# Kernel optimization log

Hardware: AMD Instinct MI355X
Metric: run time of the kernel (lower is better)

Reference implementation:

```python
import jax, jax.numpy as jnp
from jax import lax
import numpy as np

B, T, F, H, C = 2048, 200, 64, 128, 1
IN = 2 * F + H  # GRUCell input size


def setup_inputs() -> dict:
    key = jax.random.key(0)
    ks = jax.random.split(key, 16)
    sd_h = 1.0 / np.sqrt(H)
    sd_f = 1.0 / np.sqrt(F)
    sd_g = 1.0 / np.sqrt(H)
    return {
        "values": jax.random.normal(ks[0], (B, T, F), jnp.float32),
        "masks": jnp.round(jax.random.uniform(ks[1], (B, T, F), jnp.float32)),
        "deltas": jax.random.uniform(ks[2], (B, T, F), jnp.float32),
        "x_locf": jax.random.normal(ks[3], (B, T, F), jnp.float32),
        "emp_mean": jax.random.normal(ks[4], (F,), jnp.float32),
        "Wdh": jax.random.uniform(ks[5], (H, F), jnp.float32, -sd_h, sd_h),
        "bdh": jax.random.uniform(ks[6], (H,), jnp.float32, -sd_h, sd_h),
        "Wdx": jax.random.uniform(ks[7], (F, F), jnp.float32, -sd_f, sd_f),
        "bdx": jax.random.uniform(ks[8], (F,), jnp.float32, -sd_f, sd_f),
        "w_ih": jax.random.uniform(ks[9], (3 * H, IN), jnp.float32, -sd_g, sd_g),
        "w_hh": jax.random.uniform(ks[10], (3 * H, H), jnp.float32, -sd_g, sd_g),
        "b_ih": jax.random.uniform(ks[11], (3 * H,), jnp.float32, -sd_g, sd_g),
        "b_hh": jax.random.uniform(ks[12], (3 * H,), jnp.float32, -sd_g, sd_g),
        "Wc": jax.random.uniform(ks[13], (C, H), jnp.float32, -sd_g, sd_g),
        "bc": jax.random.uniform(ks[14], (C,), jnp.float32, -sd_g, sd_g),
    }


def reference(values, masks, deltas, x_locf, emp_mean,
              Wdh, bdh, Wdx, bdx, w_ih, w_hh, b_ih, b_hh, Wc, bc):
    # GRU-D forward: sequential scan over time with temporal decay gating.
    eye = jnp.eye(Wdx.shape[0], dtype=Wdx.dtype)
    Wdx_diag = Wdx * eye  # diag=True TemporalDecay

    def step(h, inp):
        x, m, d, xl = inp  # each [B, F]
        gamma_h = jnp.exp(-jax.nn.relu(d @ Wdh.T + bdh))   # [B, H]
        gamma_x = jnp.exp(-jax.nn.relu(d @ Wdx_diag.T + bdx))  # [B, F]
        h = h * gamma_h
        x_h = gamma_x * xl + (1.0 - gamma_x) * emp_mean
        x_rep = m * x + (1.0 - m) * x_h
        inputs = jnp.concatenate([x_rep, h, m], axis=1)    # [B, 2F+H]
        gi = inputs @ w_ih.T + b_ih                        # [B, 3H]
        gh = h @ w_hh.T + b_hh                             # [B, 3H]
        i_r, i_z, i_n = jnp.split(gi, 3, axis=1)
        h_r, h_z, h_n = jnp.split(gh, 3, axis=1)
        r = jax.nn.sigmoid(i_r + h_r)
        z = jax.nn.sigmoid(i_z + h_z)
        n = jnp.tanh(i_n + r * h_n)
        h_new = (1.0 - z) * n + z * h
        return h_new, None

    xs = (values.transpose(1, 0, 2), masks.transpose(1, 0, 2),
          deltas.transpose(1, 0, 2), x_locf.transpose(1, 0, 2))
    h0 = jnp.zeros((values.shape[0], Wdh.shape[0]), values.dtype)
    h_final, _ = lax.scan(step, h0, xs)
    logits = h_final @ Wc.T + bc
    return jax.nn.sigmoid(logits)
```

## Files before the change

### kernel.cpp

```cpp
#include <hip/hip_runtime.h>
#include <hip/hip_bf16.h>

#define Bsz 2048
#define Tn  200
#define Fn  64
#define Hn  128
#define INn 256
#define BBn 8

typedef __bf16 bf16x8 __attribute__((ext_vector_type(8)));
typedef float  f32x4  __attribute__((ext_vector_type(4)));

__device__ __forceinline__ float sigm(float x)  { return 1.f / (1.f + __expf(-x)); }
__device__ __forceinline__ float tanh_(float x) { return 1.f - 2.f / (__expf(2.f * x) + 1.f); }

__global__ __launch_bounds__(512, 2) void grud_scan(
    const float* __restrict__ values, const float* __restrict__ masks,
    const float* __restrict__ deltas, const float* __restrict__ x_locf,
    const float* __restrict__ emp_mean,
    const float* __restrict__ Wdh, const float* __restrict__ bdh,
    const float* __restrict__ Wdx, const float* __restrict__ bdx,
    const float* __restrict__ w_ih, const float* __restrict__ w_hh,
    const float* __restrict__ b_ih, const float* __restrict__ b_hh,
    const float* __restrict__ Wc, const float* __restrict__ bc,
    float* __restrict__ out)
{
    __shared__ __align__(16) __bf16 in_bf[16][264];
    __shared__ __align__(16) __bf16 d_bf[2][16][72];
    __shared__ float h_fin[BBn][Hn];

    const int tid  = threadIdx.x;
    const int w    = tid >> 6;
    const int lane = tid & 63;
    const int ncol = lane & 15;
    const int kg   = lane >> 4;
    const int b0   = blockIdx.x * BBn;

    for (int i = tid; i < 16 * 264;    i += 512) ((__bf16*)in_bf)[i] = (__bf16)0.f;
    for (int i = tid; i < 2 * 16 * 72; i += 512) ((__bf16*)d_bf)[i]  = (__bf16)0.f;

    bf16x8 wih[3][8], whh[3][4], wdhf[2];
    float bih_r[3], bhh_r[3];
    #pragma unroll
    for (int nt = 0; nt < 3; ++nt) {
        const int c = nt * Hn + w * 16 + ncol;
        bih_r[nt] = b_ih[c];
        bhh_r[nt] = b_hh[c];
        #pragma unroll
        for (int kc = 0; kc < 8; ++kc) {
            const float* p = w_ih + (size_t)c * INn + kc * 32 + kg * 8;
            bf16x8 v;
            #pragma unroll
            for (int e = 0; e < 8; ++e) v[e] = (__bf16)p[e];
            wih[nt][kc] = v;
        }
        #pragma unroll
        for (int kc = 0; kc < 4; ++kc) {
            const float* p = w_hh + (size_t)c * Hn + kc * 32 + kg * 8;
            bf16x8 v;
            #pragma unroll
            for (int e = 0; e < 8; ++e) v[e] = (__bf16)p[e];
            whh[nt][kc] = v;
        }
    }
    const int ch = w * 16 + ncol;
    const float bdh_r = bdh[ch];
    #pragma unroll
    for (int kc = 0; kc < 2; ++kc) {
        const float* p = Wdh + (size_t)ch * Fn + kc * 32 + kg * 8;
        bf16x8 v;
        #pragma unroll
        for (int e = 0; e < 8; ++e) v[e] = (__bf16)p[e];
        wdhf[kc] = v;
    }

    const int r_ld = w, f_ld = lane;
    const float wdxd_r = Wdx[(size_t)f_ld * Fn + f_ld];
    const float bdx_r  = bdx[f_ld];
    const float emp_r  = emp_mean[f_ld];
    const float* vp = values + (size_t)(b0 + r_ld) * Tn * Fn + f_ld;
    const float* mp = masks  + (size_t)(b0 + r_ld) * Tn * Fn + f_ld;
    const float* dp = deltas + (size_t)(b0 + r_ld) * Tn * Fn + f_ld;
    const float* lp = x_locf + (size_t)(b0 + r_ld) * Tn * Fn + f_ld;

    float h_reg[4] = {0.f, 0.f, 0.f, 0.f};

    float x_c = vp[0], m_c = mp[0], d_c = dp[0], xl_c = lp[0];
    d_bf[0][r_ld][f_ld] = (__bf16)d_c;
    __syncthreads();

    const f32x4 fz = {0.f, 0.f, 0.f, 0.f};

    for (int t = 0; t < Tn; ++t) {
        const int cur = t & 1;

        bf16x8 a0 = *(const bf16x8*)&d_bf[cur][ncol][kg * 8];
        bf16x8 a1 = *(const bf16x8*)&d_bf[cur][ncol][32 + kg * 8];
        f32x4 acc = fz;
        acc = __builtin_amdgcn_mfma_f32_16x16x32_bf16(a0, wdhf[0], acc, 0, 0, 0);
        acc = __builtin_amdgcn_mfma_f32_16x16x32_bf16(a1, wdhf[1], acc, 0, 0, 0);
        if (kg < 2) {
            #pragma unroll
            for (int i = 0; i < 4; ++i) {
                float g  = __expf(-fmaxf(acc[i] + bdh_r, 0.f));
                float hv = h_reg[i] * g;
                h_reg[i] = hv;
                in_bf[kg * 4 + i][Fn + ch] = (__bf16)hv;
            }
        }
        {
            float gx = __expf(-fmaxf(d_c * wdxd_r + bdx_r, 0.f));
            float xh = gx * xl_c + (1.f - gx) * emp_r;
            float xr = m_c * x_c + (1.f - m_c) * xh;
            in_bf[r_ld][f_ld]            = (__bf16)xr;
            in_bf[r_ld][Fn + Hn + f_ld]  = (__bf16)m_c;
        }
        const int off = (t + 1 < Tn) ? (t + 1) * Fn : t * Fn;
        float x_n = vp[off], m_n = mp[off], d_n = dp[off], xl_n = lp[off];
        __syncthreads();

        bf16x8 af[8];
        #pragma unroll
        for (int kc = 0; kc < 8; ++kc)
            af[kc] = *(const bf16x8*)&in_bf[ncol][kc * 32 + kg * 8];
        f32x4 gacc[3], hacc[3];
        #pragma unroll
        for (int nt = 0; nt < 3; ++nt) { gacc[nt] = fz; hacc[nt] = fz; }
        #pragma unroll
        for (int kc = 0; kc < 8; ++kc)
            #pragma unroll
            for (int nt = 0; nt < 3; ++nt)
                gacc[nt] = __builtin_amdgcn_mfma_f32_16x16x32_bf16(af[kc], wih[nt][kc], gacc[nt], 0, 0, 0);
        #pragma unroll
        for (int kc = 0; kc < 4; ++kc)
            #pragma unroll
            for (int nt = 0; nt < 3; ++nt)
                hacc[nt] = __builtin_amdgcn_mfma_f32_16x16x32_bf16(af[kc + 2], whh[nt][kc], hacc[nt], 0, 0, 0);
        if (kg < 2) {
            #pragma unroll
            for (int i = 0; i < 4; ++i) {
                float rg = sigm(gacc[0][i] + bih_r[0] + hacc[0][i] + bhh_r[0]);
                float zg = sigm(gacc[1][i] + bih_r[1] + hacc[1][i] + bhh_r[1]);
                float hn = hacc[2][i] + bhh_r[2];
                float ng = tanh_(gacc[2][i] + bih_r[2] + rg * hn);
                h_reg[i] = (1.f - zg) * ng + zg * h_reg[i];
            }
        }
        x_c = x_n; m_c = m_n; d_c = d_n; xl_c = xl_n;
        d_bf[cur ^ 1][r_ld][f_ld] = (__bf16)d_n;
        __syncthreads();
    }

    if (kg < 2) {
        #pragma unroll
        for (int i = 0; i < 4; ++i) h_fin[kg * 4 + i][ch] = h_reg[i];
    }
    __syncthreads();
    if (tid < BBn) {
        float acc = bc[0];
        #pragma unroll 8
        for (int j = 0; j < Hn; ++j) acc += h_fin[tid][j] * Wc[j];
        out[b0 + tid] = sigm(acc);
    }
}

extern "C" void kernel_launch(void* const* d_in, const int* in_sizes, int n_in,
                              void* d_out, int out_size, void* d_ws, size_t ws_size,
                              hipStream_t stream)
{
    (void)in_sizes; (void)n_in; (void)out_size; (void)d_ws; (void)ws_size;
    grud_scan<<<dim3(Bsz / BBn), dim3(512), 0, stream>>>(
        (const float*)d_in[0],  (const float*)d_in[1],  (const float*)d_in[2],
        (const float*)d_in[3],  (const float*)d_in[4],  (const float*)d_in[5],
        (const float*)d_in[6],  (const float*)d_in[7],  (const float*)d_in[8],
        (const float*)d_in[9],  (const float*)d_in[10], (const float*)d_in[11],
        (const float*)d_in[12], (const float*)d_in[13], (const float*)d_in[14],
        (float*)d_out);
}
```

Measured before the change: 621.5 us.

## Fold W_hh r/z weights into W_ih and double-buffer LDS to drop a barrier

Because h appears in both the input concatenation and the hidden matmul, the r and z rows of w_hh are pre-added into the matching w_ih columns. This removes eight MFMAs per step, and only the n-gate hidden product stays separate. The input tile is double-buffered and the decay matmul for the next step is computed one step ahead, so each iteration needs one barrier instead of two. Summing weights before the bf16 conversion changes rounding slightly, and the single-barrier scheme relies on careful buffer alternation.

```diff
diff --git a/kernel.cpp b/kernel.cpp
--- a/kernel.cpp
+++ b/kernel.cpp
@@ -25,7 +25,7 @@
     const float* __restrict__ Wc, const float* __restrict__ bc,
     float* __restrict__ out)
 {
-    __shared__ __align__(16) __bf16 in_bf[16][264];
+    __shared__ __align__(16) __bf16 in_bf[2][16][264];
     __shared__ __align__(16) __bf16 d_bf[2][16][72];
     __shared__ float h_fin[BBn][Hn];
 
@@ -36,10 +36,10 @@
     const int kg   = lane >> 4;
     const int b0   = blockIdx.x * BBn;
 
-    for (int i = tid; i < 16 * 264;    i += 512) ((__bf16*)in_bf)[i] = (__bf16)0.f;
-    for (int i = tid; i < 2 * 16 * 72; i += 512) ((__bf16*)d_bf)[i]  = (__bf16)0.f;
+    for (int i = tid; i < 2 * 16 * 264; i += 512) ((__bf16*)in_bf)[i] = (__bf16)0.f;
+    for (int i = tid; i < 2 * 16 * 72;  i += 512) ((__bf16*)d_bf)[i]  = (__bf16)0.f;
 
-    bf16x8 wih[3][8], whh[3][4], wdhf[2];
+    bf16x8 wih[3][8], whn[4], wdhf[2];
     float bih_r[3], bhh_r[3];
     #pragma unroll
     for (int nt = 0; nt < 3; ++nt) {
@@ -49,18 +49,23 @@
         #pragma unroll
         for (int kc = 0; kc < 8; ++kc) {
             const float* p = w_ih + (size_t)c * INn + kc * 32 + kg * 8;
+            const bool fold = (nt < 2) & (kc >= 2) & (kc < 6);
+            const float* q = w_hh + (size_t)c * Hn + (kc - 2) * 32 + kg * 8;
             bf16x8 v;
             #pragma unroll
-            for (int e = 0; e < 8; ++e) v[e] = (__bf16)p[e];
+            for (int e = 0; e < 8; ++e) v[e] = (__bf16)(p[e] + (fold ? q[e] : 0.f));
             wih[nt][kc] = v;
         }
+    }
+    {
+        const int cn = 2 * Hn + w * 16 + ncol;
         #pragma unroll
         for (int kc = 0; kc < 4; ++kc) {
-            const float* p = w_hh + (size_t)c * Hn + kc * 32 + kg * 8;
+            const float* q = w_hh + (size_t)cn * Hn + kc * 32 + kg * 8;
             bf16x8 v;
             #pragma unroll
-            for (int e = 0; e < 8; ++e) v[e] = (__bf16)p[e];
-            whh[nt][kc] = v;
+            for (int e = 0; e < 8; ++e) v[e] = (__bf16)q[e];
+            whn[kc] = v;
         }
     }
     const int ch = w * 16 + ncol;
@@ -73,6 +78,8 @@
         for (int e = 0; e < 8; ++e) v[e] = (__bf16)p[e];
         wdhf[kc] = v;
     }
+    const float bs0 = bih_r[0] + bhh_r[0];
+    const float bs1 = bih_r[1] + bhh_r[1];
 
     const int r_ld = w, f_ld = lane;
     const float wdxd_r = Wdx[(size_t)f_ld * Fn + f_ld];
@@ -84,48 +91,60 @@
     const float* lp = x_locf + (size_t)(b0 + r_ld) * Tn * Fn + f_ld;
 
     float h_reg[4] = {0.f, 0.f, 0.f, 0.f};
-
-    float x_c = vp[0], m_c = mp[0], d_c = dp[0], xl_c = lp[0];
-    d_bf[0][r_ld][f_ld] = (__bf16)d_c;
-    __syncthreads();
-
     const f32x4 fz = {0.f, 0.f, 0.f, 0.f};
 
+    float x_c = vp[0], m_c = mp[0], xl_c = lp[0];
+    float d_cur = dp[0];
+    float d_w   = dp[Fn];
+    d_bf[1][r_ld][f_ld] = (__bf16)d_cur;
+    __syncthreads();
+    f32x4 gam = fz;
+    {
+        bf16x8 g0 = *(const bf16x8*)&d_bf[1][ncol][kg * 8];
+        bf16x8 g1 = *(const bf16x8*)&d_bf[1][ncol][32 + kg * 8];
+        gam = __builtin_amdgcn_mfma_f32_16x16x32_bf16(g0, wdhf[0], gam, 0, 0, 0);
+        gam = __builtin_amdgcn_mfma_f32_16x16x32_bf16(g1, wdhf[1], gam, 0, 0, 0);
+    }
+
     for (int t = 0; t < Tn; ++t) {
-        const int cur = t & 1;
+        const int buf = t & 1;
 
-        bf16x8 a0 = *(const bf16x8*)&d_bf[cur][ncol][kg * 8];
-        bf16x8 a1 = *(const bf16x8*)&d_bf[cur][ncol][32 + kg * 8];
-        f32x4 acc = fz;
-        acc = __builtin_amdgcn_mfma_f32_16x16x32_bf16(a0, wdhf[0], acc, 0, 0, 0);
-        acc = __builtin_amdgcn_mfma_f32_16x16x32_bf16(a1, wdhf[1], acc, 0, 0, 0);
+        const int o1 = (t + 1 < Tn ? t + 1 : Tn - 1) * Fn;
+        const int o2 = (t + 2 < Tn ? t + 2 : Tn - 1) * Fn;
+        const float x_n = vp[o1], m_n = mp[o1], xl_n = lp[o1], d_nn = dp[o2];
+
         if (kg < 2) {
             #pragma unroll
             for (int i = 0; i < 4; ++i) {
-                float g  = __expf(-fmaxf(acc[i] + bdh_r, 0.f));
-                float hv = h_reg[i] * g;
-                h_reg[i] = hv;
-                in_bf[kg * 4 + i][Fn + ch] = (__bf16)hv;
+                float g = __expf(-fmaxf(gam[i] + bdh_r, 0.f));
+                h_reg[i] *= g;
+                in_bf[buf][kg * 4 + i][Fn + ch] = (__bf16)h_reg[i];
             }
         }
         {
-            float gx = __expf(-fmaxf(d_c * wdxd_r + bdx_r, 0.f));
+            float gx = __expf(-fmaxf(d_cur * wdxd_r + bdx_r, 0.f));
             float xh = gx * xl_c + (1.f - gx) * emp_r;
             float xr = m_c * x_c + (1.f - m_c) * xh;
-            in_bf[r_ld][f_ld]            = (__bf16)xr;
-            in_bf[r_ld][Fn + Hn + f_ld]  = (__bf16)m_c;
+            in_bf[buf][r_ld][f_ld]           = (__bf16)xr;
+            in_bf[buf][r_ld][Fn + Hn + f_ld] = (__bf16)m_c;
+            d_bf[buf][r_ld][f_ld]            = (__bf16)d_w;
         }
-        const int off = (t + 1 < Tn) ? (t + 1) * Fn : t * Fn;
-        float x_n = vp[off], m_n = mp[off], d_n = dp[off], xl_n = lp[off];
-        __syncthreads();
+        asm volatile("s_waitcnt lgkmcnt(0)" ::: "memory");
+        __builtin_amdgcn_s_barrier();
+
+        f32x4 gnew = fz;
+        {
+            bf16x8 g0 = *(const bf16x8*)&d_bf[buf][ncol][kg * 8];
+            bf16x8 g1 = *(const bf16x8*)&d_bf[buf][ncol][32 + kg * 8];
+            gnew = __builtin_amdgcn_mfma_f32_16x16x32_bf16(g0, wdhf[0], gnew, 0, 0, 0);
+            gnew = __builtin_amdgcn_mfma_f32_16x16x32_bf16(g1, wdhf[1], gnew, 0, 0, 0);
+        }
 
         bf16x8 af[8];
         #pragma unroll
         for (int kc = 0; kc < 8; ++kc)
-            af[kc] = *(const bf16x8*)&in_bf[ncol][kc * 32 + kg * 8];
-        f32x4 gacc[3], hacc[3];
-        #pragma unroll
-        for (int nt = 0; nt < 3; ++nt) { gacc[nt] = fz; hacc[nt] = fz; }
+            af[kc] = *(const bf16x8*)&in_bf[buf][ncol][kc * 32 + kg * 8];
+        f32x4 gacc[3] = {fz, fz, fz}, nacc = fz;
         #pragma unroll
         for (int kc = 0; kc < 8; ++kc)
             #pragma unroll
@@ -133,22 +152,21 @@
                 gacc[nt] = __builtin_amdgcn_mfma_f32_16x16x32_bf16(af[kc], wih[nt][kc], gacc[nt], 0, 0, 0);
         #pragma unroll
         for (int kc = 0; kc < 4; ++kc)
-            #pragma unroll
-            for (int nt = 0; nt < 3; ++nt)
-                hacc[nt] = __builtin_amdgcn_mfma_f32_16x16x32_bf16(af[kc + 2], whh[nt][kc], hacc[nt], 0, 0, 0);
+            nacc = __builtin_amdgcn_mfma_f32_16x16x32_bf16(af[kc + 2], whn[kc], nacc, 0, 0, 0);
+
         if (kg < 2) {
             #pragma unroll
             for (int i = 0; i < 4; ++i) {
-                float rg = sigm(gacc[0][i] + bih_r[0] + hacc[0][i] + bhh_r[0]);
-                float zg = sigm(gacc[1][i] + bih_r[1] + hacc[1][i] + bhh_r[1]);
-                float hn = hacc[2][i] + bhh_r[2];
+                float rg = sigm(gacc[0][i] + bs0);
+                float zg = sigm(gacc[1][i] + bs1);
+                float hn = nacc[i] + bhh_r[2];
                 float ng = tanh_(gacc[2][i] + bih_r[2] + rg * hn);
                 h_reg[i] = (1.f - zg) * ng + zg * h_reg[i];
             }
         }
-        x_c = x_n; m_c = m_n; d_c = d_n; xl_c = xl_n;
-        d_bf[cur ^ 1][r_ld][f_ld] = (__bf16)d_n;
-        __syncthreads();
+        gam = gnew;
+        x_c = x_n; m_c = m_n; xl_c = xl_n;
+        d_cur = d_w; d_w = d_nn;
     }
 
     if (kg < 2) {
```

Measured after the change: 574.0 us. -7.7%, faster.
